# Kernel tuning notes

Measured on AMD Instinct MI355X. Metric: run time of the kernel, lower is better.

## Reference

```python
import jax, jax.numpy as jnp
import numpy as np

FEAT = 1024
SUPPORT = 512
N = 4096


def setup_inputs() -> dict:
    key = jax.random.key(0)
    k1, k2, k3, k4, k5, k6 = jax.random.split(key, 6)
    s = 1.0 / np.sqrt(FEAT)
    f = jax.random.normal(k1, (N, FEAT), dtype=jnp.float32)
    G = jax.random.normal(k2, (SUPPORT, FEAT), dtype=jnp.float32)
    # PyTorch LSTMCell params: weight_ih [4*hidden, input], weight_hh [4*hidden, hidden]
    W_ih = jax.random.uniform(k3, (4 * FEAT, 2 * FEAT), minval=-s, maxval=s, dtype=jnp.float32)
    W_hh = jax.random.uniform(k4, (4 * FEAT, FEAT), minval=-s, maxval=s, dtype=jnp.float32)
    b_ih = jax.random.uniform(k5, (4 * FEAT,), minval=-s, maxval=s, dtype=jnp.float32)
    b_hh = jax.random.uniform(k6, (4 * FEAT,), minval=-s, maxval=s, dtype=jnp.float32)
    return {"f": f, "G": G, "W_ih": W_ih, "W_hh": W_hh, "b_ih": b_ih, "b_hh": b_hh, "n_ways": 20}


def _lstm_cell(x, h, c, W_ih, W_hh, b_ih, b_hh):
    # gates ordered i, f, g, o as in torch.nn.LSTMCell
    gates = x @ W_ih.T + b_ih + h @ W_hh.T + b_hh  # [N, 4*FEAT]
    i, fg, g, o = jnp.split(gates, 4, axis=1)
    i = jax.nn.sigmoid(i)
    fg = jax.nn.sigmoid(fg)
    g = jnp.tanh(g)
    o = jax.nn.sigmoid(o)
    c_new = fg * c + i * g
    h_new = o * jnp.tanh(c_new)
    return h_new, c_new


def reference(f, G, W_ih, W_hh, b_ih, b_hh, n_ways):
    h = f
    c = jnp.zeros_like(f)  # c_0 expanded, zeros (non-learned Variable)
    for _ in range(n_ways):
        logit_a = h @ G.T                      # [N, M]
        a = jax.nn.softmax(logit_a, axis=0)    # softmax over dim 0, as in original
        r = a @ G                              # [N, FEAT]
        x = jnp.concatenate((f, r), axis=1)    # [N, 2*FEAT]
        h, c = _lstm_cell(x, h, c, W_ih, W_hh, b_ih, b_hh)
        h = h + f
    return h
```

## Files before the change

kernel.cpp:

```cpp
#include <hip/hip_runtime.h>
#include <math.h>

#define NB    4096
#define FEAT  1024
#define MSUP  512
#define G4    4096
#define NWAYS 20

typedef _Float16 f16;
typedef f16 f16x8 __attribute__((ext_vector_type(8)));
typedef f16 f16x4 __attribute__((ext_vector_type(4)));
typedef float f32x4 __attribute__((ext_vector_type(4)));
typedef unsigned int u32;
#define GLOBAL_AS __attribute__((address_space(1)))
#define LDS_AS    __attribute__((address_space(3)))

__device__ __forceinline__ void load_lds16(const void* g, void* l) {
    __builtin_amdgcn_global_load_lds((const GLOBAL_AS u32*)g, (LDS_AS u32*)l, 16, 0, 0);
}

__device__ __forceinline__ float sigm(float x) { return 1.f / (1.f + __expf(-x)); }

template<int BM, int BN, int WROWS, int WCOLS, bool OUTF16, bool HASBIAS>
__global__ __launch_bounds__(256) void mfma_nt(
    void* __restrict__ Cv, int ldc,
    const f16* __restrict__ A1, int lda1, const f16* __restrict__ B1, int ldb1, int K1,
    const f16* __restrict__ A2, int lda2, const f16* __restrict__ B2, int ldb2, int K2,
    const f16* __restrict__ A3, int lda3, const f16* __restrict__ B3, int ldb3, int K3,
    const float* __restrict__ bias)
{
    constexpr int BK = 32;
    constexpr int WM = BM / WROWS, WN = BN / WCOLS;
    constexpr int FM = WM / 16,   FN = WN / 16;
    __shared__ f16 As[BM][BK];
    __shared__ f16 Bs[BN][BK];
    const int tid  = threadIdx.x;
    const int lane = tid & 63;
    const int wrow = (tid >> 6) % WROWS, wcol = (tid >> 6) / WROWS;
    const int bm = blockIdx.y * BM, bn = blockIdx.x * BN;
    const int lr = lane & 15, lq = lane >> 4;

    f32x4 acc[FM][FN] = {};

    #pragma unroll
    for (int pass = 0; pass < 3; ++pass) {
        const f16* A = pass == 0 ? A1 : (pass == 1 ? A2 : A3);
        const f16* B = pass == 0 ? B1 : (pass == 1 ? B2 : B3);
        const int lda = pass == 0 ? lda1 : (pass == 1 ? lda2 : lda3);
        const int ldb = pass == 0 ? ldb1 : (pass == 1 ? ldb2 : ldb3);
        const int K   = pass == 0 ? K1  : (pass == 1 ? K2  : K3);
        if (!A) break;
        #pragma unroll 1
        for (int k0 = 0; k0 < K; k0 += BK) {
            __syncthreads();
            #pragma unroll
            for (int t = 0; t < (BM * 4) / 256; ++t) {
                int c = t * 256 + tid;
                load_lds16(A + (size_t)(bm + (c >> 2)) * lda + k0 + (c & 3) * 8,
                           &As[0][0] + ((size_t)t * 256 + (tid & 192)) * 8);
            }
            #pragma unroll
            for (int t = 0; t < (BN * 4) / 256; ++t) {
                int c = t * 256 + tid;
                load_lds16(B + (size_t)(bn + (c >> 2)) * ldb + k0 + (c & 3) * 8,
                           &Bs[0][0] + ((size_t)t * 256 + (tid & 192)) * 8);
            }
            __syncthreads();
            f16x8 af[FM], bf[FN];
            #pragma unroll
            for (int i = 0; i < FM; ++i)
                af[i] = *(const f16x8*)&As[wrow * WM + i * 16 + lr][lq * 8];
            #pragma unroll
            for (int j = 0; j < FN; ++j)
                bf[j] = *(const f16x8*)&Bs[wcol * WN + j * 16 + lr][lq * 8];
            #pragma unroll
            for (int i = 0; i < FM; ++i)
                #pragma unroll
                for (int j = 0; j < FN; ++j)
                    acc[i][j] = __builtin_amdgcn_mfma_f32_16x16x32_f16(af[i], bf[j], acc[i][j], 0, 0, 0);
        }
    }

    #pragma unroll
    for (int i = 0; i < FM; ++i) {
        #pragma unroll
        for (int j = 0; j < FN; ++j) {
            const int col  = bn + wcol * WN + j * 16 + lr;
            const int row0 = bm + wrow * WM + i * 16 + lq * 4;
            float badd = HASBIAS ? bias[col] : 0.f;
            #pragma unroll
            for (int r = 0; r < 4; ++r) {
                size_t off = (size_t)(row0 + r) * ldc + col;
                float v = acc[i][j][r] + badd;
                if (OUTF16) ((f16*)Cv)[off] = (f16)v;
                else        ((float*)Cv)[off] = v;
            }
        }
    }
}

template<int DUMMY>
__global__ __launch_bounds__(256, 2) void gates_mp(
    const f16* __restrict__ a,
    const f16* __restrict__ h,
    const f16* __restrict__ Wcat,
    const f16* __restrict__ pre,
    const float* __restrict__ fin,
    float* __restrict__ cbuf,
    f16* __restrict__ hh,
    float* __restrict__ hout,
    int first, int writeH)
{
    extern __shared__ f16x8 smem8[];
    f16* smem = (f16*)smem8;
    const int tid  = threadIdx.x;
    const int lane = tid & 63;
    const int wid  = tid >> 6;
    const int wrow = wid >> 1, wcol = wid & 1;
    const int lr = lane & 15, lq = lane >> 4;

    const int bidr = blockIdx.y * 32 + blockIdx.x;
    const int wg   = (bidr & 7) * 128 + (bidr >> 3);
    const int bm = (wg >> 5) * 128;
    const int bn = (wg & 31) * 128;

    f32x4 acc[4][4] = {};

    auto stage = [&](const f16* src, int ld, int rb, int ko, f16* lbase, int l) {
        int c = l * 256 + tid;
        int r = c >> 3;
        int x = (c & 7) ^ (r & 7);
        load_lds16(src + (size_t)(rb + r) * ld + ko + (x << 3),
                   lbase + ((size_t)(l * 256 + (tid & 192))) * 8);
    };
    #define RDF(BUF, RB, KK) \
        (*(const f16x8*)((BUF) + ((size_t)((RB) + lr) << 6) + ((((KK) << 2 | lq) ^ (lr & 7)) << 3)))

    #pragma unroll
    for (int l = 0; l < 4; ++l) {
        stage(a,    MSUP, bm, 0, smem,        l);
        stage(Wcat, 2048, bn, 0, smem + 8192, l);
    }
    __syncthreads();

    #pragma unroll 1
    for (int t = 0; t < 32; ++t) {
        f16* Ab = smem + (t & 1) * 16384;
        f16* Bb = Ab + 8192;
        f16* An = smem + ((t + 1) & 1) * 16384;
        f16* Bn = An + 8192;
        const int k1 = (t + 1) * 64;
        const f16* As2 = a; int lda2 = MSUP, ko2 = k1;
        if (k1 >= 1024)     { As2 = h; lda2 = FEAT; ko2 = k1 - 1024; }
        else if (k1 >= 512) { ko2 = k1 - 512; }

        f16x8 af[4][2], bf[4][2];
        #pragma unroll
        for (int i = 0; i < 4; ++i)
            #pragma unroll
            for (int kk = 0; kk < 2; ++kk)
                af[i][kk] = RDF(Ab, wrow * 64 + i * 16, kk);
        #pragma unroll
        for (int j = 0; j < 4; ++j)
            #pragma unroll
            for (int kk = 0; kk < 2; ++kk)
                bf[j][kk] = RDF(Bb, wcol * 64 + j * 16, kk);

        if (t < 31) {
            #pragma unroll
            for (int l = 0; l < 4; ++l) {
                stage(As2, lda2, bm, ko2, An, l);
                stage(Wcat, 2048, bn, k1, Bn, l);
            }
        }

        #pragma unroll
        for (int kk = 0; kk < 2; ++kk)
            #pragma unroll
            for (int i = 0; i < 4; ++i)
                #pragma unroll
                for (int j = 0; j < 4; ++j)
                    acc[i][j] = __builtin_amdgcn_mfma_f32_16x16x32_f16(af[i][kk], bf[j][kk], acc[i][j], 0, 0, 0);

        __syncthreads();
    }
    #undef RDF

    const int q  = lane & 3;
    const int fk = (lane >> 2) & 3;
    #pragma unroll
    for (int i = 0; i < 4; ++i) {
        #pragma unroll
        for (int j = 0; j < 4; ++j) {
            const int cb   = bn + wcol * 64 + j * 16;
            const int row0 = bm + wrow * 64 + i * 16 + lq * 4;
            float x[4];
            #pragma unroll
            for (int r = 0; r < 4; ++r) x[r] = acc[i][j][r];
            float g4[4];
            #pragma unroll
            for (int k = 0; k < 4; ++k) {
                int srcq = (q + k) & 3;
                int src  = (lane & ~3) | srcq;
                g4[srcq] = __shfl(x[(q - k + 4) & 3], src, 64);
            }
            const int row  = row0 + q;
            const int feat = (cb >> 2) + fk;
            f16x4 p = *(const f16x4*)(pre + (size_t)row * G4 + cb + 4 * fk);
            const float i_ = sigm(g4[0] + (float)p[0]);
            const float f_ = sigm(g4[1] + (float)p[1]);
            const float g_ = tanhf(g4[2] + (float)p[2]);
            const float o_ = sigm(g4[3] + (float)p[3]);
            const size_t cid = ((size_t)(blockIdx.y * gridDim.x + blockIdx.x) * 16
                                + i * 4 + j) * 256 + tid;
            float cold = first ? 0.f : cbuf[cid];
            float cn = i_ * g_ + f_ * cold;
            cbuf[cid] = cn;
            float hn = o_ * tanhf(cn) + fin[(size_t)row * FEAT + feat];
            hh[(size_t)row * FEAT + feat] = (f16)hn;
            if (writeH) hout[(size_t)row * FEAT + feat] = hn;
        }
    }
}

__global__ __launch_bounds__(256) void softmax_rows_kernel(
    const float* __restrict__ X, f16* __restrict__ Y)
{
    const int row = blockIdx.x;
    const float* x = X + (size_t)row * NB;
    f16* y = Y + (size_t)row * NB;
    const int tid = threadIdx.x;
    float v[16];
    float mx = -1e30f;
    #pragma unroll
    for (int i = 0; i < 16; ++i) { v[i] = x[tid + (i << 8)]; mx = fmaxf(mx, v[i]); }
    #pragma unroll
    for (int off = 32; off > 0; off >>= 1) mx = fmaxf(mx, __shfl_down(mx, off));
    __shared__ float sm[4];
    if ((tid & 63) == 0) sm[tid >> 6] = mx;
    __syncthreads();
    mx = fmaxf(fmaxf(sm[0], sm[1]), fmaxf(sm[2], sm[3]));
    float s = 0.f;
    #pragma unroll
    for (int i = 0; i < 16; ++i) { v[i] = __expf(v[i] - mx); s += v[i]; }
    #pragma unroll
    for (int off = 32; off > 0; off >>= 1) s += __shfl_down(s, off);
    __shared__ float ss[4];
    if ((tid & 63) == 0) ss[tid >> 6] = s;
    __syncthreads();
    s = ss[0] + ss[1] + ss[2] + ss[3];
    const float inv = 1.f / s;
    #pragma unroll
    for (int i = 0; i < 16; ++i) y[tid + (i << 8)] = (f16)(v[i] * inv);
}

__global__ __launch_bounds__(256) void transpose_f16_kernel(
    const f16* __restrict__ in, f16* __restrict__ out, int R, int C)
{
    __shared__ f16 t[64][65];
    const int r0 = blockIdx.y * 64, c0 = blockIdx.x * 64;
    const int lr = threadIdx.x & 63, lw = threadIdx.x >> 6;
    #pragma unroll
    for (int i = 0; i < 16; ++i) {
        int rr = lw * 16 + i;
        t[rr][lr] = in[(size_t)(r0 + rr) * C + c0 + lr];
    }
    __syncthreads();
    #pragma unroll
    for (int i = 0; i < 16; ++i) {
        int cc = lw * 16 + i;
        out[(size_t)(c0 + cc) * R + r0 + lr] = t[lr][cc];
    }
}

__global__ __launch_bounds__(256) void cvt_f16_kernel(
    const float* __restrict__ in, f16* __restrict__ out, int n)
{
    int idx = (blockIdx.x * 256 + threadIdx.x) * 4;
    if (idx < n) {
        float4 v = *(const float4*)(in + idx);
        f16x4 o = {(f16)v.x, (f16)v.y, (f16)v.z, (f16)v.w};
        *(f16x4*)(out + idx) = o;
    }
}

__global__ __launch_bounds__(256) void cvt_perm_kernel(
    const float* __restrict__ in, f16* __restrict__ out, int ld_in, int ld_out, int col_off)
{
    int idx = (blockIdx.x * 256 + threadIdx.x) * 4;
    int j = idx / ld_in, k = idx % ld_in;
    int dst = 4 * (j & 1023) + (j >> 10);
    float4 v = *(const float4*)(in + idx);
    f16x4 o = {(f16)v.x, (f16)v.y, (f16)v.z, (f16)v.w};
    *(f16x4*)(out + (size_t)dst * ld_out + col_off + k) = o;
}

__global__ __launch_bounds__(256) void bias_perm_kernel(
    const float* __restrict__ bih, const float* __restrict__ bhh, float* __restrict__ out)
{
    int j = blockIdx.x * 256 + threadIdx.x;
    out[4 * (j & 1023) + (j >> 10)] = bih[j] + bhh[j];
}

__global__ __launch_bounds__(256) void split_wcat_kernel(
    const float* __restrict__ in, f16* __restrict__ out)
{
    int idx = (blockIdx.x * 256 + threadIdx.x) * 4;
    int g = idx >> 9, k = idx & 511;
    float4 v = *(const float4*)(in + idx);
    f16x4 hi = {(f16)v.x, (f16)v.y, (f16)v.z, (f16)v.w};
    f16x4 lo = {(f16)(v.x - (float)hi.x), (f16)(v.y - (float)hi.y),
                (f16)(v.z - (float)hi.z), (f16)(v.w - (float)hi.w)};
    *(f16x4*)(out + (size_t)g * 2048 + k) = hi;
    *(f16x4*)(out + (size_t)g * 2048 + 512 + k) = lo;
}

extern "C" void kernel_launch(void* const* d_in, const int* in_sizes, int n_in,
                              void* d_out, int out_size, void* d_ws, size_t ws_size,
                              hipStream_t stream) {
    const float* f   = (const float*)d_in[0];
    const float* G   = (const float*)d_in[1];
    const float* Wih = (const float*)d_in[2];
    const float* Whh = (const float*)d_in[3];
    const float* bih = (const float*)d_in[4];
    const float* bhh = (const float*)d_in[5];
    float* h = (float*)d_out;

    char* W = (char*)d_ws;
    f16*   pre_h   = (f16*)(W);
    float* aT      = (float*)(W + (size_t)(32 << 20));
    f16*   aTh     = (f16*)(W + (size_t)(40 << 20));
    f16*   a_h     = (f16*)(W + (size_t)(44 << 20));
    float* cbuf    = (float*)(W + (size_t)(48 << 20));
    f16*   h0      = (f16*)(W + (size_t)(64 << 20));
    f16*   hA      = (f16*)(W + (size_t)(72 << 20));
    f16*   hB      = (f16*)(W + (size_t)(80 << 20));
    f16*   Wih_h   = (f16*)(W + (size_t)(88 << 20));
    f16*   Wcat    = (f16*)(W + (size_t)(104 << 20));
    float* Wr32    = (float*)(W + (size_t)(120 << 20));
    f16*   G_h     = (f16*)(W + (size_t)(128 << 20));
    float* bias_p  = (float*)(W + (size_t)(129 << 20));

    const f16* NF = nullptr;
    const dim3 blk(256);

    hipFuncSetAttribute((const void*)gates_mp<0>,
                        hipFuncAttributeMaxDynamicSharedMemorySize, 65536);

    cvt_f16_kernel<<<(NB * FEAT) / 1024, blk, 0, stream>>>(f, h0, NB * FEAT);
    cvt_perm_kernel<<<(G4 * 2 * FEAT) / 1024, blk, 0, stream>>>(Wih, Wih_h, 2 * FEAT, 2 * FEAT, 0);
    cvt_perm_kernel<<<(G4 * FEAT) / 1024, blk, 0, stream>>>(Whh, Wcat, FEAT, 2048, 1024);
    cvt_f16_kernel<<<(MSUP * FEAT) / 1024, blk, 0, stream>>>(G, G_h, MSUP * FEAT);
    bias_perm_kernel<<<G4 / 256, blk, 0, stream>>>(bih, bhh, bias_p);

    mfma_nt<128, 128, 2, 2, true, true><<<dim3(G4 / 128, NB / 128), blk, 0, stream>>>(
        pre_h, G4,
        h0, FEAT, Wih_h, 2 * FEAT, FEAT,
        NF, 0, NF, 0, 0, NF, 0, NF, 0, 0,
        bias_p);

    mfma_nt<128, 128, 2, 2, false, false><<<dim3(MSUP / 128, G4 / 128), blk, 0, stream>>>(
        Wr32, MSUP,
        Wih_h + FEAT, 2 * FEAT, G_h, FEAT, FEAT,
        NF, 0, NF, 0, 0, NF, 0, NF, 0, 0,
        nullptr);
    split_wcat_kernel<<<(G4 * MSUP) / 1024, blk, 0, stream>>>(Wr32, Wcat);

    const f16* hcur = h0;
    for (int it = 0; it < NWAYS; ++it) {
        mfma_nt<64, 64, 2, 2, false, false><<<dim3(NB / 64, MSUP / 64), blk, 0, stream>>>(
            aT, NB,
            G_h, FEAT, hcur, FEAT, FEAT,
            NF, 0, NF, 0, 0, NF, 0, NF, 0, 0,
            nullptr);

        softmax_rows_kernel<<<MSUP, blk, 0, stream>>>(aT, aTh);
        transpose_f16_kernel<<<dim3(NB / 64, MSUP / 64), blk, 0, stream>>>(aTh, a_h, MSUP, NB);

        f16* hnext = (it & 1) ? hB : hA;
        gates_mp<0><<<dim3(32, 32), 256, 65536, stream>>>(
            a_h, hcur, Wcat, pre_h, f, cbuf, hnext, h, it == 0, it == NWAYS - 1);
        hcur = hnext;
    }
}
```

Before: 2.632 ms.

## Replace double-buffered 64-K gates GEMM with single-buffered 32-K tiles in static LDS

The fused gates kernel drops its double-buffered 64-wide K pipeline in 64KB dynamic LDS. It now uses single-buffered 32-wide K tiles in 16KB of static shared memory with a sync before and after each load. Occupancy is raised to 3 blocks per SM so other resident blocks can hide load latency. In exchange there is no prefetch overlap within a block, twice as many barriers, and a lower MFMA-to-sync ratio.

After: 2.520 ms. 4.3% less time.

```diff
diff --git a/kernel.cpp b/kernel.cpp
--- a/kernel.cpp
+++ b/kernel.cpp
@@ -99,8 +99,7 @@
     }
 }
 
-template<int DUMMY>
-__global__ __launch_bounds__(256, 2) void gates_mp(
+__global__ __launch_bounds__(256, 3) void gates_m97(
     const f16* __restrict__ a,
     const f16* __restrict__ h,
     const f16* __restrict__ Wcat,
@@ -111,8 +110,8 @@
     float* __restrict__ hout,
     int first, int writeH)
 {
-    extern __shared__ f16x8 smem8[];
-    f16* smem = (f16*)smem8;
+    __shared__ f16 As[128][32];
+    __shared__ f16 Bs[128][32];
     const int tid  = threadIdx.x;
     const int lane = tid & 63;
     const int wid  = tid >> 6;
@@ -126,65 +125,43 @@
 
     f32x4 acc[4][4] = {};
 
+    const int rr4 = tid >> 2;
+    const int xx4 = ((tid & 3) ^ (rr4 & 3)) << 3;
     auto stage = [&](const f16* src, int ld, int rb, int ko, f16* lbase, int l) {
-        int c = l * 256 + tid;
-        int r = c >> 3;
-        int x = (c & 7) ^ (r & 7);
-        load_lds16(src + (size_t)(rb + r) * ld + ko + (x << 3),
+        load_lds16(src + (size_t)(rb + l * 64 + rr4) * ld + ko + xx4,
                    lbase + ((size_t)(l * 256 + (tid & 192))) * 8);
     };
-    #define RDF(BUF, RB, KK) \
-        (*(const f16x8*)((BUF) + ((size_t)((RB) + lr) << 6) + ((((KK) << 2 | lq) ^ (lr & 7)) << 3)))
-
-    #pragma unroll
-    for (int l = 0; l < 4; ++l) {
-        stage(a,    MSUP, bm, 0, smem,        l);
-        stage(Wcat, 2048, bn, 0, smem + 8192, l);
-    }
-    __syncthreads();
 
     #pragma unroll 1
-    for (int t = 0; t < 32; ++t) {
-        f16* Ab = smem + (t & 1) * 16384;
-        f16* Bb = Ab + 8192;
-        f16* An = smem + ((t + 1) & 1) * 16384;
-        f16* Bn = An + 8192;
-        const int k1 = (t + 1) * 64;
-        const f16* As2 = a; int lda2 = MSUP, ko2 = k1;
-        if (k1 >= 1024)     { As2 = h; lda2 = FEAT; ko2 = k1 - 1024; }
-        else if (k1 >= 512) { ko2 = k1 - 512; }
-
-        f16x8 af[4][2], bf[4][2];
+    for (int k0 = 0; k0 < 2048; k0 += 32) {
+        const f16* Asrc = a; int lda = MSUP, ko = k0;
+        if (k0 >= 1024)     { Asrc = h; lda = FEAT; ko = k0 - 1024; }
+        else if (k0 >= 512) { ko = k0 - 512; }
+
+        __syncthreads();
+        stage(Asrc, lda, bm, ko, &As[0][0], 0);
+        stage(Asrc, lda, bm, ko, &As[0][0], 1);
+        stage(Wcat, 2048, bn, k0, &Bs[0][0], 0);
+        stage(Wcat, 2048, bn, k0, &Bs[0][0], 1);
+        __syncthreads();
+
+        f16x8 af[4], bf[4];
+        #pragma unroll
+        for (int i = 0; i < 4; ++i) {
+            int r = wrow * 64 + i * 16 + lr;
+            af[i] = *(const f16x8*)&As[r][(lq ^ (lr & 3)) * 8];
+        }
+        #pragma unroll
+        for (int j = 0; j < 4; ++j) {
+            int r = wcol * 64 + j * 16 + lr;
+            bf[j] = *(const f16x8*)&Bs[r][(lq ^ (lr & 3)) * 8];
+        }
         #pragma unroll
         for (int i = 0; i < 4; ++i)
             #pragma unroll
-            for (int kk = 0; kk < 2; ++kk)
-                af[i][kk] = RDF(Ab, wrow * 64 + i * 16, kk);
-        #pragma unroll
-        for (int j = 0; j < 4; ++j)
-            #pragma unroll
-            for (int kk = 0; kk < 2; ++kk)
-                bf[j][kk] = RDF(Bb, wcol * 64 + j * 16, kk);
-
-        if (t < 31) {
-            #pragma unroll
-            for (int l = 0; l < 4; ++l) {
-                stage(As2, lda2, bm, ko2, An, l);
-                stage(Wcat, 2048, bn, k1, Bn, l);
-            }
-        }
-
-        #pragma unroll
-        for (int kk = 0; kk < 2; ++kk)
-            #pragma unroll
-            for (int i = 0; i < 4; ++i)
-                #pragma unroll
-                for (int j = 0; j < 4; ++j)
-                    acc[i][j] = __builtin_amdgcn_mfma_f32_16x16x32_f16(af[i][kk], bf[j][kk], acc[i][j], 0, 0, 0);
-
-        __syncthreads();
-    }
-    #undef RDF
+            for (int j = 0; j < 4; ++j)
+                acc[i][j] = __builtin_amdgcn_mfma_f32_16x16x32_f16(af[i], bf[j], acc[i][j], 0, 0, 0);
+    }
 
     const int q  = lane & 3;
     const int fk = (lane >> 2) & 3;
@@ -344,9 +321,6 @@
     const f16* NF = nullptr;
     const dim3 blk(256);
 
-    hipFuncSetAttribute((const void*)gates_mp<0>,
-                        hipFuncAttributeMaxDynamicSharedMemorySize, 65536);
-
     cvt_f16_kernel<<<(NB * FEAT) / 1024, blk, 0, stream>>>(f, h0, NB * FEAT);
     cvt_perm_kernel<<<(G4 * 2 * FEAT) / 1024, blk, 0, stream>>>(Wih, Wih_h, 2 * FEAT, 2 * FEAT, 0);
     cvt_perm_kernel<<<(G4 * FEAT) / 1024, blk, 0, stream>>>(Whh, Wcat, FEAT, 2048, 1024);
@@ -378,7 +352,7 @@
         transpose_f16_kernel<<<dim3(NB / 64, MSUP / 64), blk, 0, stream>>>(aTh, a_h, MSUP, NB);
 
         f16* hnext = (it & 1) ? hB : hA;
-        gates_mp<0><<<dim3(32, 32), 256, 65536, stream>>>(
+        gates_m97<<<dim3(32, 32), blk, 0, stream>>>(
             a_h, hcur, Wcat, pre_h, f, cbuf, hnext, h, it == 0, it == NWAYS - 1);
         hcur = hnext;
     }
```
